# Optimization experiments

Measured on AMD Instinct MI355X. Metric: run time of the kernel, lower is better.

## Reference

```python
import jax, jax.numpy as jnp
import numpy as np

N = 4194304   # variable nodes
M = 2097152   # check nodes
DC = 10       # max check degree


def setup_inputs() -> dict:
    key = jax.random.key(0)
    k1, k2 = jax.random.split(key)
    cn_adj = jax.random.randint(k1, (M, DC), 0, N, dtype=jnp.int32)
    # pad: last neighbor slot of every other check is empty (-1)
    cn_adj = cn_adj.at[:, -1].set(jnp.where(jnp.arange(M) % 2 == 0, -1, cn_adj[:, -1]))
    llr0 = jax.random.normal(k2, (N,), jnp.float32)
    gamma = jnp.ones((), jnp.float32)  # learnable scaling (learn_gamma=True)
    return {"llr0": llr0, "gamma": gamma, "cn_adj": cn_adj, "n_iter": 5}


def _bp(llr0, gamma, cn_adj, n_iter):
    n = llr0.shape[0]
    valid = cn_adj >= 0
    # original gathers v2c[cn_adj] with raw -1 entries -> numpy-style wrap to index n-1
    gather_idx = jnp.where(valid, cn_adj, n - 1)
    # original masks padded slots out of the scatter-add only
    scatter_idx = jnp.where(valid, cn_adj, 0)

    def bp_step(v2c, _):
        msgs = v2c[gather_idx]                               # (M, DC) gather
        sign = jnp.prod(jnp.sign(msgs + 1e-12), axis=1)      # (M,)
        mag = jnp.min(jnp.abs(msgs), axis=1)                 # (M,) min-sum magnitude
        c2v = gamma * sign * mag                             # (M,) scaled min-sum
        msg = jnp.where(valid, c2v[:, None], 0.0)            # mask padded edges
        v_sum = jnp.zeros(n, llr0.dtype).at[scatter_idx].add(msg)  # scatter-add to variables
        return llr0 + v_sum - v2c, None

    v2c0 = jnp.zeros(n, llr0.dtype)
    v2c_final, _ = jax.lax.scan(bp_step, v2c0, None, length=n_iter)
    return llr0 + v2c_final


def reference(llr0, gamma, cn_adj, n_iter):
    return _bp(llr0, gamma, cn_adj, n_iter)
```

## Files before the change

kernel.cpp:

```cpp
#include <hip/hip_runtime.h>
#include <hip/hip_fp16.h>

#define DCC 10
#define NB 2048
#define NBLK 256
#define HTHREADS 1024

typedef int iv4 __attribute__((ext_vector_type(4)));


__global__ __launch_bounds__(256) void bp_init2_kernel(
    const float* __restrict__ llr0, float* __restrict__ v2c,
    unsigned short* __restrict__ v2c_h, int Nq) {
  int i = blockIdx.x * blockDim.x + threadIdx.x;
  if (i >= Nq) return;
  float4 l = reinterpret_cast<const float4*>(llr0)[i];
  reinterpret_cast<float4*>(v2c)[i] = l;
  reinterpret_cast<__half2*>(v2c_h)[2 * i]     = __floats2half2_rn(l.x, l.y);
  reinterpret_cast<__half2*>(v2c_h)[2 * i + 1] = __floats2half2_rn(l.z, l.w);
}

__global__ __launch_bounds__(HTHREADS) void bp_hist_kernel(
    const int* __restrict__ adj, unsigned* __restrict__ hist,
    int i4_per_block, int i4_total) {
  __shared__ unsigned h[NB];
  for (int i = threadIdx.x; i < NB; i += HTHREADS) h[i] = 0u;
  __syncthreads();
  const iv4* p = reinterpret_cast<const iv4*>(adj);
  int base = blockIdx.x * i4_per_block;
  int lim = base + i4_per_block;
  if (lim > i4_total) lim = i4_total;
  for (int g = base + (int)threadIdx.x; g < lim; g += HTHREADS) {
    iv4 r = __builtin_nontemporal_load(p + g);
    if (r.x >= 0) atomicAdd(&h[(unsigned)r.x >> 11], 1u);
    if (r.y >= 0) atomicAdd(&h[(unsigned)r.y >> 11], 1u);
    if (r.z >= 0) atomicAdd(&h[(unsigned)r.z >> 11], 1u);
    if (r.w >= 0) atomicAdd(&h[(unsigned)r.w >> 11], 1u);
  }
  __syncthreads();
  for (int i = threadIdx.x; i < NB; i += HTHREADS)
    hist[(size_t)i * NBLK + blockIdx.x] = h[i];
}

__global__ __launch_bounds__(256) void bp_scan1_kernel(
    unsigned* __restrict__ data, unsigned* __restrict__ sums) {
  __shared__ unsigned ts[256];
  const int base = blockIdx.x * 1024;
  uint4 d = reinterpret_cast<const uint4*>(data + base)[threadIdx.x];
  unsigned tsum = d.x + d.y + d.z + d.w;
  ts[threadIdx.x] = tsum;
  __syncthreads();
  for (int off = 1; off < 256; off <<= 1) {
    unsigned add = ((int)threadIdx.x >= off) ? ts[threadIdx.x - off] : 0u;
    __syncthreads();
    ts[threadIdx.x] += add;
    __syncthreads();
  }
  unsigned run = ts[threadIdx.x] - tsum;
  if (threadIdx.x == 255) sums[blockIdx.x] = ts[255];
  uint4 o;
  o.x = run; run += d.x;
  o.y = run; run += d.y;
  o.z = run; run += d.z;
  o.w = run;
  reinterpret_cast<uint4*>(data + base)[threadIdx.x] = o;
}

__global__ __launch_bounds__(256) void bp_scan2_kernel(
    unsigned* __restrict__ sums, unsigned* __restrict__ total_p, int n) {
  __shared__ unsigned ts[256];
  __shared__ unsigned carry_s;
  if (threadIdx.x == 0) carry_s = 0u;
  __syncthreads();
  for (int c = 0; c < n; c += 256) {
    int idx = c + (int)threadIdx.x;
    unsigned orig = (idx < n) ? sums[idx] : 0u;
    ts[threadIdx.x] = orig;
    __syncthreads();
    for (int off = 1; off < 256; off <<= 1) {
      unsigned add = ((int)threadIdx.x >= off) ? ts[threadIdx.x - off] : 0u;
      __syncthreads();
      ts[threadIdx.x] += add;
      __syncthreads();
    }
    unsigned excl = ts[threadIdx.x] - orig + carry_s;
    if (idx < n) sums[idx] = excl;
    __syncthreads();
    if (threadIdx.x == 0) carry_s += ts[255];
    __syncthreads();
  }
  if (threadIdx.x == 0) *total_p = carry_s;
}

__global__ __launch_bounds__(HTHREADS) void bp_sortscatter_kernel(
    const int* __restrict__ adj, const unsigned* __restrict__ hist_s,
    const unsigned* __restrict__ sums_s, unsigned* __restrict__ recs,
    int i4_per_block, int i4_total) {
  __shared__ unsigned gstart[NB];
  __shared__ unsigned cnt[NB];
  __shared__ unsigned flushed[NB];
  __shared__ unsigned buf[NB * 8];
  for (int i = threadIdx.x; i < NB; i += HTHREADS) {
    unsigned idx = (unsigned)i * NBLK + blockIdx.x;
    gstart[i] = hist_s[idx] + sums_s[idx >> 10];
    cnt[i] = 0u;
    flushed[i] = 0u;
  }
  __syncthreads();
  const iv4* p = reinterpret_cast<const iv4*>(adj);
  int base = blockIdx.x * i4_per_block;
  int lim = base + i4_per_block;
  if (lim > i4_total) lim = i4_total;
  for (int ph = base; ph < lim; ph += HTHREADS) {
    int g = ph + (int)threadIdx.x;
    if (g < lim) {
      iv4 r = __builtin_nontemporal_load(p + g);
      int s4 = g * 4;
      int av[4] = {r.x, r.y, r.z, r.w};
#pragma unroll
      for (int j = 0; j < 4; ++j) {
        int ai = av[j];
        if (ai >= 0) {
          unsigned bin = (unsigned)ai >> 11;
          unsigned rec =
              ((unsigned)(ai & (NB - 1)) << 21) | ((unsigned)(s4 + j) / DCC);
          unsigned pos = atomicAdd(&cnt[bin], 1u);
          if (pos < flushed[bin] + 8u)
            buf[bin * 8 + (pos & 7u)] = rec;
          else
            recs[gstart[bin] + pos] = rec;
        }
      }
    }
    __syncthreads();
    for (int b = threadIdx.x; b < NB; b += HTHREADS) {
      unsigned c = cnt[b], f = flushed[b];
      if (c - f >= 8u) {
        unsigned gp = gstart[b] + f;
#pragma unroll
        for (int k = 0; k < 8; ++k) recs[gp + k] = buf[b * 8 + ((f + k) & 7u)];
        flushed[b] = c;
      }
    }
    __syncthreads();
  }
  for (int b = threadIdx.x; b < NB; b += HTHREADS) {
    unsigned c = cnt[b], f = flushed[b], gp = gstart[b];
    for (unsigned q = f; q < c; ++q) recs[gp + q] = buf[b * 8 + (q & 7u)];
  }
}

__global__ __launch_bounds__(256) void bp_gather1_kernel(
    const int* __restrict__ adj, const unsigned short* __restrict__ v2c_h,
    unsigned* __restrict__ state, int Mhalf, int N, int lo, int hi) {
  int t = blockIdx.x * blockDim.x + threadIdx.x;
  if (t >= Mhalf) return;
  const iv4* p = reinterpret_cast<const iv4*>(adj + (size_t)t * 2 * DCC);
  iv4 r0 = __builtin_nontemporal_load(p);
  iv4 r1 = __builtin_nontemporal_load(p + 1);
  iv4 r2 = __builtin_nontemporal_load(p + 2);
  iv4 r3 = __builtin_nontemporal_load(p + 3);
  iv4 r4 = __builtin_nontemporal_load(p + 4);
  int a[20] = {r0.x, r0.y, r0.z, r0.w, r1.x, r1.y, r1.z, r1.w,
               r2.x, r2.y, r2.z, r2.w, r3.x, r3.y, r3.z, r3.w,
               r4.x, r4.y, r4.z, r4.w};
  unsigned s2[2];
#pragma unroll
  for (int c = 0; c < 2; ++c) {
    unsigned sgn = 0u;
    unsigned mab = 0x7c00u;
#pragma unroll
    for (int j = 0; j < DCC; ++j) {
      int ai = a[c * DCC + j];
      int gi = (ai >= 0) ? ai : (N - 1);
      if (gi >= lo && gi < hi) {
        unsigned hb = (unsigned)v2c_h[gi];
        unsigned ab = hb & 0x7fffu;
        sgn ^= (ab != 0u) ? (hb & 0x8000u) : 0u;
        mab = (ab < mab) ? ab : mab;
      }
    }
    s2[c] = mab | sgn;
  }
  state[t] = s2[0] | (s2[1] << 16);
}

__global__ __launch_bounds__(256) void bp_gather2_kernel(
    const int* __restrict__ adj, const unsigned short* __restrict__ v2c_h,
    const unsigned* __restrict__ state0, unsigned short* __restrict__ c2v_h,
    const float* __restrict__ gamma_p, int Mhalf, int N, int lo, int hi) {
  int t = blockIdx.x * blockDim.x + threadIdx.x;
  if (t >= Mhalf) return;
  const float gamma = *gamma_p;
  const iv4* p = reinterpret_cast<const iv4*>(adj + (size_t)t * 2 * DCC);
  iv4 r0 = __builtin_nontemporal_load(p);
  iv4 r1 = __builtin_nontemporal_load(p + 1);
  iv4 r2 = __builtin_nontemporal_load(p + 2);
  iv4 r3 = __builtin_nontemporal_load(p + 3);
  iv4 r4 = __builtin_nontemporal_load(p + 4);
  int a[20] = {r0.x, r0.y, r0.z, r0.w, r1.x, r1.y, r1.z, r1.w,
               r2.x, r2.y, r2.z, r2.w, r3.x, r3.y, r3.z, r3.w,
               r4.x, r4.y, r4.z, r4.w};
  unsigned p0 = state0[t];
  unsigned outw = 0u;
#pragma unroll
  for (int c = 0; c < 2; ++c) {
    unsigned sgn = 0u;
    unsigned mab = 0x7c00u;
#pragma unroll
    for (int j = 0; j < DCC; ++j) {
      int ai = a[c * DCC + j];
      int gi = (ai >= 0) ? ai : (N - 1);
      if (gi >= lo && gi < hi) {
        unsigned hb = (unsigned)v2c_h[gi];
        unsigned ab = hb & 0x7fffu;
        sgn ^= (ab != 0u) ? (hb & 0x8000u) : 0u;
        mab = (ab < mab) ? ab : mab;
      }
    }
    unsigned q0 = (c == 0) ? (p0 & 0xffffu) : (p0 >> 16);
    unsigned a0 = q0 & 0x7fffu;
    unsigned ab = (a0 < mab) ? a0 : mab;
    unsigned sg = ((q0 ^ sgn) & 0x8000u);
    float val = gamma * __half2float(__ushort_as_half((unsigned short)ab));
    val = __uint_as_float(__float_as_uint(val) ^ (sg << 16));
    outw |= ((unsigned)__half_as_ushort(__float2half_rn(val))) << (16 * c);
  }
  reinterpret_cast<unsigned*>(c2v_h)[t] = outw;
}

__global__ __launch_bounds__(256) void bp_accvar_kernel(
    const unsigned* __restrict__ recs, const unsigned short* __restrict__ c2v_h,
    const unsigned* __restrict__ hist_s, const unsigned* __restrict__ sums_s,
    const unsigned* __restrict__ total_p, const float* __restrict__ llr0,
    float* __restrict__ v2c, unsigned short* __restrict__ v2c_h,
    float* __restrict__ out) {
  __shared__ __align__(16) float acc[NB];
  const int b = blockIdx.x;
  for (int i = threadIdx.x; i < NB; i += 256) acc[i] = 0.0f;
  unsigned i0 = (unsigned)b * NBLK;
  unsigned start = hist_s[i0] + sums_s[i0 >> 10];
  unsigned end = (b == NB - 1)
                     ? *total_p
                     : (hist_s[i0 + NBLK] + sums_s[(i0 + NBLK) >> 10]);
  __syncthreads();
  for (unsigned e = start + threadIdx.x; e < end; e += 256) {
    unsigned rec = recs[e];
    float val = __half2float(__ushort_as_half(c2v_h[rec & 0x1FFFFFu]));
    atomicAdd(&acc[rec >> 21], val);
  }
  __syncthreads();
  const int gq = b * (NB / 4);
#pragma unroll
  for (int k = 0; k < 2; ++k) {
    int li = k * 256 + (int)threadIdx.x;
    int gi = gq + li;
    float4 l = reinterpret_cast<const float4*>(llr0)[gi];
    float4 v = reinterpret_cast<float4*>(v2c)[gi];
    float4 s = reinterpret_cast<const float4*>(acc)[li];
    float4 nv;
    nv.x = l.x + s.x - v.x;
    nv.y = l.y + s.y - v.y;
    nv.z = l.z + s.z - v.z;
    nv.w = l.w + s.w - v.w;
    if (out != nullptr) {
      float4 o;
      o.x = l.x + nv.x;
      o.y = l.y + nv.y;
      o.z = l.z + nv.z;
      o.w = l.w + nv.w;
      reinterpret_cast<float4*>(out)[gi] = o;
    } else {
      reinterpret_cast<float4*>(v2c)[gi] = nv;
      reinterpret_cast<__half2*>(v2c_h)[2 * gi]     = __floats2half2_rn(nv.x, nv.y);
      reinterpret_cast<__half2*>(v2c_h)[2 * gi + 1] = __floats2half2_rn(nv.z, nv.w);
    }
  }
}


__global__ __launch_bounds__(256) void bp_init_kernel(
    const float* __restrict__ llr0, float* __restrict__ v2c,
    float* __restrict__ vsum, __half* __restrict__ v2c_h, int Nq) {
  int i = blockIdx.x * blockDim.x + threadIdx.x;
  if (i >= Nq) return;
  float4 l = reinterpret_cast<const float4*>(llr0)[i];
  reinterpret_cast<float4*>(v2c)[i] = l;
  reinterpret_cast<float4*>(vsum)[i] = make_float4(0.f, 0.f, 0.f, 0.f);
  reinterpret_cast<__half2*>(v2c_h)[2 * i]     = __floats2half2_rn(l.x, l.y);
  reinterpret_cast<__half2*>(v2c_h)[2 * i + 1] = __floats2half2_rn(l.z, l.w);
}

__global__ __launch_bounds__(256) void bp_check_kernel(
    const int* __restrict__ adj, const __half* __restrict__ v2c_h,
    float* __restrict__ vsum, const float* __restrict__ gamma_p,
    int Mhalf, int N) {
  int t = blockIdx.x * blockDim.x + threadIdx.x;
  if (t >= Mhalf) return;
  const float gamma = *gamma_p;
  const int4* p = reinterpret_cast<const int4*>(adj + (size_t)t * 2 * DCC);
  int4 r0 = p[0], r1 = p[1], r2 = p[2], r3 = p[3], r4 = p[4];
  int a[20] = {r0.x, r0.y, r0.z, r0.w, r1.x, r1.y, r1.z, r1.w,
               r2.x, r2.y, r2.z, r2.w, r3.x, r3.y, r3.z, r3.w,
               r4.x, r4.y, r4.z, r4.w};
#pragma unroll
  for (int c = 0; c < 2; ++c) {
    unsigned sgnbits = 0u;
    float mag = 3.402823466e+38f;
#pragma unroll
    for (int j = 0; j < DCC; ++j) {
      int ai = a[c * DCC + j];
      int gi = (ai >= 0) ? ai : (N - 1);
      float v = __half2float(v2c_h[gi]);
      sgnbits ^= (__float_as_uint(v + 1e-12f) & 0x80000000u);
      mag = fminf(mag, fabsf(v));
    }
    float c2v = __uint_as_float(__float_as_uint(gamma * mag) ^ sgnbits);
#pragma unroll
    for (int j = 0; j < DCC; ++j) {
      int ai = a[c * DCC + j];
      if (ai >= 0) unsafeAtomicAdd(&vsum[ai], c2v);
    }
  }
}

__global__ __launch_bounds__(256) void bp_var_kernel(
    const float* __restrict__ llr0, float* __restrict__ v2c,
    float* __restrict__ vsum, __half* __restrict__ v2c_h,
    float* __restrict__ out, int Nq) {
  int i = blockIdx.x * blockDim.x + threadIdx.x;
  if (i >= Nq) return;
  float4 l = reinterpret_cast<const float4*>(llr0)[i];
  float4 v = reinterpret_cast<float4*>(v2c)[i];
  float4 s = reinterpret_cast<float4*>(vsum)[i];
  float4 nv;
  nv.x = l.x + s.x - v.x;
  nv.y = l.y + s.y - v.y;
  nv.z = l.z + s.z - v.z;
  nv.w = l.w + s.w - v.w;
  reinterpret_cast<float4*>(v2c)[i] = nv;
  reinterpret_cast<float4*>(vsum)[i] = make_float4(0.f, 0.f, 0.f, 0.f);
  reinterpret_cast<__half2*>(v2c_h)[2 * i]     = __floats2half2_rn(nv.x, nv.y);
  reinterpret_cast<__half2*>(v2c_h)[2 * i + 1] = __floats2half2_rn(nv.z, nv.w);
  if (out != nullptr) {
    float4 o;
    o.x = l.x + nv.x;
    o.y = l.y + nv.y;
    o.z = l.z + nv.z;
    o.w = l.w + nv.w;
    reinterpret_cast<float4*>(out)[i] = o;
  }
}


extern "C" void kernel_launch(void* const* d_in, const int* in_sizes, int n_in,
                              void* d_out, int out_size, void* d_ws, size_t ws_size,
                              hipStream_t stream) {
  const float* llr0  = (const float*)d_in[0];
  const float* gamma = (const float*)d_in[1];
  const int*   adj   = (const int*)d_in[2];
  const int N = in_sizes[0];
  const int M = in_sizes[2] / DCC;
  const int Mh = M / 2;
  const int NITER = 5;
  const int Nq = N / 4;
  const int varBlocks = (Nq + 255) / 256;
  const int chkBlocks = (Mh + 255) / 256;
  const int Nh = N / 2;

  char* w = (char*)d_ws;
  auto carve = [&](size_t bytes) {
    char* r = w;
    w += (bytes + 255) & ~(size_t)255;
    return r;
  };
  float*          v2c    = (float*)carve((size_t)N * 4);
  unsigned short* v2c_h  = (unsigned short*)carve((size_t)N * 2);
  unsigned*       state0 = (unsigned*)carve((size_t)Mh * 4);
  unsigned short* c2v_h  = (unsigned short*)carve((size_t)M * 2);
  unsigned*       hist   = (unsigned*)carve((size_t)NB * NBLK * 4);
  unsigned*       sums   = (unsigned*)carve((size_t)513 * 4);
  unsigned*       recs   = (unsigned*)carve((size_t)M * DCC * 4);
  unsigned*       total_p = sums + 512;
  size_t need = (size_t)(w - (char*)d_ws);

  const int i4_total = (M * DCC) / 4;
  const int i4_per_block = (i4_total + NBLK - 1) / NBLK;
  const int scanN = (NB * NBLK) / 1024;

  bool fast = (need <= ws_size) && (N == NB * 2048) && (M <= (1 << 21)) &&
              ((M * DCC) % 4 == 0);

  if (fast) {
    bp_init2_kernel<<<varBlocks, 256, 0, stream>>>(llr0, v2c, v2c_h, Nq);
    bp_hist_kernel<<<NBLK, HTHREADS, 0, stream>>>(adj, hist, i4_per_block, i4_total);
    bp_scan1_kernel<<<scanN, 256, 0, stream>>>(hist, sums);
    bp_scan2_kernel<<<1, 256, 0, stream>>>(sums, total_p, scanN);
    bp_sortscatter_kernel<<<NBLK, HTHREADS, 0, stream>>>(adj, hist, sums, recs,
                                                         i4_per_block, i4_total);
    for (int it = 1; it < NITER; ++it) {
      bp_gather1_kernel<<<chkBlocks, 256, 0, stream>>>(
          adj, v2c_h, state0, Mh, N, 0, Nh);
      bp_gather2_kernel<<<chkBlocks, 256, 0, stream>>>(
          adj, v2c_h, state0, c2v_h, gamma, Mh, N, Nh, N);
      float* outp = (it == NITER - 1) ? (float*)d_out : nullptr;
      bp_accvar_kernel<<<NB, 256, 0, stream>>>(
          recs, c2v_h, hist, sums, total_p, llr0, v2c, v2c_h, outp);
    }
  } else {
    float*  fv2c   = (float*)d_ws;
    float*  fvsum  = fv2c + N;
    __half* fv2c_h = (__half*)(fvsum + N);
    bp_init_kernel<<<varBlocks, 256, 0, stream>>>(llr0, fv2c, fvsum, fv2c_h, Nq);
    for (int it = 1; it < NITER; ++it) {
      bp_check_kernel<<<chkBlocks, 256, 0, stream>>>(adj, fv2c_h, fvsum, gamma, Mh, N);
      float* outp = (it == NITER - 1) ? (float*)d_out : nullptr;
      bp_var_kernel<<<varBlocks, 256, 0, stream>>>(llr0, fv2c, fvsum, fv2c_h, outp, Nq);
    }
  }
}
```

Before: 1.337 ms.

## Process four checks per thread, privatize histogram, widen sort buffers

The gather kernels now handle four check nodes per thread instead of two. Each thread loads ten int4 adjacency vectors and writes uint2 state and c2v words, which means fewer threads and wider stores. The histogram kernel splits its shared bins by thread parity to reduce atomic contention. The sort-scatter kernel doubles its per-bin staging buffer to 16 entries and rotates slots by bin index, aiming for longer coalesced flushes and fewer LDS bank conflicts. In exchange, the gather kernels use more registers per thread and fewer threads are available to hide gather latency.

```diff
diff --git a/kernel.cpp b/kernel.cpp
--- a/kernel.cpp
+++ b/kernel.cpp
@@ -23,23 +23,24 @@
 __global__ __launch_bounds__(HTHREADS) void bp_hist_kernel(
     const int* __restrict__ adj, unsigned* __restrict__ hist,
     int i4_per_block, int i4_total) {
-  __shared__ unsigned h[NB];
-  for (int i = threadIdx.x; i < NB; i += HTHREADS) h[i] = 0u;
-  __syncthreads();
+  __shared__ unsigned h[2 * NB];
+  for (int i = threadIdx.x; i < 2 * NB; i += HTHREADS) h[i] = 0u;
+  __syncthreads();
+  const unsigned par = threadIdx.x & 1u;
   const iv4* p = reinterpret_cast<const iv4*>(adj);
   int base = blockIdx.x * i4_per_block;
   int lim = base + i4_per_block;
   if (lim > i4_total) lim = i4_total;
   for (int g = base + (int)threadIdx.x; g < lim; g += HTHREADS) {
     iv4 r = __builtin_nontemporal_load(p + g);
-    if (r.x >= 0) atomicAdd(&h[(unsigned)r.x >> 11], 1u);
-    if (r.y >= 0) atomicAdd(&h[(unsigned)r.y >> 11], 1u);
-    if (r.z >= 0) atomicAdd(&h[(unsigned)r.z >> 11], 1u);
-    if (r.w >= 0) atomicAdd(&h[(unsigned)r.w >> 11], 1u);
+    if (r.x >= 0) atomicAdd(&h[(((unsigned)r.x >> 11) << 1) | par], 1u);
+    if (r.y >= 0) atomicAdd(&h[(((unsigned)r.y >> 11) << 1) | par], 1u);
+    if (r.z >= 0) atomicAdd(&h[(((unsigned)r.z >> 11) << 1) | par], 1u);
+    if (r.w >= 0) atomicAdd(&h[(((unsigned)r.w >> 11) << 1) | par], 1u);
   }
   __syncthreads();
   for (int i = threadIdx.x; i < NB; i += HTHREADS)
-    hist[(size_t)i * NBLK + blockIdx.x] = h[i];
+    hist[(size_t)i * NBLK + blockIdx.x] = h[2 * i] + h[2 * i + 1];
 }
 
 __global__ __launch_bounds__(256) void bp_scan1_kernel(
@@ -99,7 +100,7 @@
   __shared__ unsigned gstart[NB];
   __shared__ unsigned cnt[NB];
   __shared__ unsigned flushed[NB];
-  __shared__ unsigned buf[NB * 8];
+  __shared__ unsigned buf[NB * 16];
   for (int i = threadIdx.x; i < NB; i += HTHREADS) {
     unsigned idx = (unsigned)i * NBLK + blockIdx.x;
     gstart[i] = hist_s[idx] + sums_s[idx >> 10];
@@ -125,8 +126,8 @@
           unsigned rec =
               ((unsigned)(ai & (NB - 1)) << 21) | ((unsigned)(s4 + j) / DCC);
           unsigned pos = atomicAdd(&cnt[bin], 1u);
-          if (pos < flushed[bin] + 8u)
-            buf[bin * 8 + (pos & 7u)] = rec;
+          if (pos < flushed[bin] + 16u)
+            buf[bin * 16 + ((pos + bin) & 15u)] = rec;
           else
             recs[gstart[bin] + pos] = rec;
         }
@@ -135,10 +136,11 @@
     __syncthreads();
     for (int b = threadIdx.x; b < NB; b += HTHREADS) {
       unsigned c = cnt[b], f = flushed[b];
-      if (c - f >= 8u) {
+      if (c - f >= 16u) {
         unsigned gp = gstart[b] + f;
 #pragma unroll
-        for (int k = 0; k < 8; ++k) recs[gp + k] = buf[b * 8 + ((f + k) & 7u)];
+        for (int k = 0; k < 16; ++k)
+          recs[gp + k] = buf[b * 16 + ((f + k + b) & 15u)];
         flushed[b] = c;
       }
     }
@@ -146,27 +148,26 @@
   }
   for (int b = threadIdx.x; b < NB; b += HTHREADS) {
     unsigned c = cnt[b], f = flushed[b], gp = gstart[b];
-    for (unsigned q = f; q < c; ++q) recs[gp + q] = buf[b * 8 + (q & 7u)];
+    for (unsigned q = f; q < c; ++q)
+      recs[gp + q] = buf[b * 16 + ((q + b) & 15u)];
   }
 }
 
 __global__ __launch_bounds__(256) void bp_gather1_kernel(
     const int* __restrict__ adj, const unsigned short* __restrict__ v2c_h,
-    unsigned* __restrict__ state, int Mhalf, int N, int lo, int hi) {
+    uint2* __restrict__ state, int Mq, int N, int lo, int hi) {
   int t = blockIdx.x * blockDim.x + threadIdx.x;
-  if (t >= Mhalf) return;
-  const iv4* p = reinterpret_cast<const iv4*>(adj + (size_t)t * 2 * DCC);
-  iv4 r0 = __builtin_nontemporal_load(p);
-  iv4 r1 = __builtin_nontemporal_load(p + 1);
-  iv4 r2 = __builtin_nontemporal_load(p + 2);
-  iv4 r3 = __builtin_nontemporal_load(p + 3);
-  iv4 r4 = __builtin_nontemporal_load(p + 4);
-  int a[20] = {r0.x, r0.y, r0.z, r0.w, r1.x, r1.y, r1.z, r1.w,
-               r2.x, r2.y, r2.z, r2.w, r3.x, r3.y, r3.z, r3.w,
-               r4.x, r4.y, r4.z, r4.w};
-  unsigned s2[2];
-#pragma unroll
-  for (int c = 0; c < 2; ++c) {
+  if (t >= Mq) return;
+  const iv4* p = reinterpret_cast<const iv4*>(adj + (size_t)t * 4 * DCC);
+  int a[40];
+#pragma unroll
+  for (int k = 0; k < 10; ++k) {
+    iv4 r = __builtin_nontemporal_load(p + k);
+    a[4 * k] = r.x; a[4 * k + 1] = r.y; a[4 * k + 2] = r.z; a[4 * k + 3] = r.w;
+  }
+  unsigned s4[4];
+#pragma unroll
+  for (int c = 0; c < 4; ++c) {
     unsigned sgn = 0u;
     unsigned mab = 0x7c00u;
 #pragma unroll
@@ -180,31 +181,30 @@
         mab = (ab < mab) ? ab : mab;
       }
     }
-    s2[c] = mab | sgn;
-  }
-  state[t] = s2[0] | (s2[1] << 16);
+    s4[c] = mab | sgn;
+  }
+  state[t] = make_uint2(s4[0] | (s4[1] << 16), s4[2] | (s4[3] << 16));
 }
 
 __global__ __launch_bounds__(256) void bp_gather2_kernel(
     const int* __restrict__ adj, const unsigned short* __restrict__ v2c_h,
-    const unsigned* __restrict__ state0, unsigned short* __restrict__ c2v_h,
-    const float* __restrict__ gamma_p, int Mhalf, int N, int lo, int hi) {
+    const uint2* __restrict__ state0, unsigned short* __restrict__ c2v_h,
+    const float* __restrict__ gamma_p, int Mq, int N, int lo, int hi) {
   int t = blockIdx.x * blockDim.x + threadIdx.x;
-  if (t >= Mhalf) return;
+  if (t >= Mq) return;
   const float gamma = *gamma_p;
-  const iv4* p = reinterpret_cast<const iv4*>(adj + (size_t)t * 2 * DCC);
-  iv4 r0 = __builtin_nontemporal_load(p);
-  iv4 r1 = __builtin_nontemporal_load(p + 1);
-  iv4 r2 = __builtin_nontemporal_load(p + 2);
-  iv4 r3 = __builtin_nontemporal_load(p + 3);
-  iv4 r4 = __builtin_nontemporal_load(p + 4);
-  int a[20] = {r0.x, r0.y, r0.z, r0.w, r1.x, r1.y, r1.z, r1.w,
-               r2.x, r2.y, r2.z, r2.w, r3.x, r3.y, r3.z, r3.w,
-               r4.x, r4.y, r4.z, r4.w};
-  unsigned p0 = state0[t];
-  unsigned outw = 0u;
-#pragma unroll
-  for (int c = 0; c < 2; ++c) {
+  const iv4* p = reinterpret_cast<const iv4*>(adj + (size_t)t * 4 * DCC);
+  int a[40];
+#pragma unroll
+  for (int k = 0; k < 10; ++k) {
+    iv4 r = __builtin_nontemporal_load(p + k);
+    a[4 * k] = r.x; a[4 * k + 1] = r.y; a[4 * k + 2] = r.z; a[4 * k + 3] = r.w;
+  }
+  uint2 p0 = state0[t];
+  unsigned q4[4] = {p0.x & 0xffffu, p0.x >> 16, p0.y & 0xffffu, p0.y >> 16};
+  unsigned ow[4];
+#pragma unroll
+  for (int c = 0; c < 4; ++c) {
     unsigned sgn = 0u;
     unsigned mab = 0x7c00u;
 #pragma unroll
@@ -218,15 +218,16 @@
         mab = (ab < mab) ? ab : mab;
       }
     }
-    unsigned q0 = (c == 0) ? (p0 & 0xffffu) : (p0 >> 16);
+    unsigned q0 = q4[c];
     unsigned a0 = q0 & 0x7fffu;
     unsigned ab = (a0 < mab) ? a0 : mab;
     unsigned sg = ((q0 ^ sgn) & 0x8000u);
     float val = gamma * __half2float(__ushort_as_half((unsigned short)ab));
     val = __uint_as_float(__float_as_uint(val) ^ (sg << 16));
-    outw |= ((unsigned)__half_as_ushort(__float2half_rn(val))) << (16 * c);
-  }
-  reinterpret_cast<unsigned*>(c2v_h)[t] = outw;
+    ow[c] = (unsigned)__half_as_ushort(__float2half_rn(val));
+  }
+  reinterpret_cast<uint2*>(c2v_h)[t] =
+      make_uint2(ow[0] | (ow[1] << 16), ow[2] | (ow[3] << 16));
 }
 
 __global__ __launch_bounds__(256) void bp_accvar_kernel(
@@ -362,10 +363,11 @@
   const int N = in_sizes[0];
   const int M = in_sizes[2] / DCC;
   const int Mh = M / 2;
+  const int Mq4 = M / 4;
   const int NITER = 5;
   const int Nq = N / 4;
   const int varBlocks = (Nq + 255) / 256;
-  const int chkBlocks = (Mh + 255) / 256;
+  const int chkBlocks4 = (Mq4 + 255) / 256;
   const int Nh = N / 2;
 
   char* w = (char*)d_ws;
@@ -389,7 +391,7 @@
   const int scanN = (NB * NBLK) / 1024;
 
   bool fast = (need <= ws_size) && (N == NB * 2048) && (M <= (1 << 21)) &&
-              ((M * DCC) % 4 == 0);
+              ((M % 4) == 0) && ((M * DCC) % 4 == 0);
 
   if (fast) {
     bp_init2_kernel<<<varBlocks, 256, 0, stream>>>(llr0, v2c, v2c_h, Nq);
@@ -399,10 +401,10 @@
     bp_sortscatter_kernel<<<NBLK, HTHREADS, 0, stream>>>(adj, hist, sums, recs,
                                                          i4_per_block, i4_total);
     for (int it = 1; it < NITER; ++it) {
-      bp_gather1_kernel<<<chkBlocks, 256, 0, stream>>>(
-          adj, v2c_h, state0, Mh, N, 0, Nh);
-      bp_gather2_kernel<<<chkBlocks, 256, 0, stream>>>(
-          adj, v2c_h, state0, c2v_h, gamma, Mh, N, Nh, N);
+      bp_gather1_kernel<<<chkBlocks4, 256, 0, stream>>>(
+          adj, v2c_h, (uint2*)state0, Mq4, N, 0, Nh);
+      bp_gather2_kernel<<<chkBlocks4, 256, 0, stream>>>(
+          adj, v2c_h, (const uint2*)state0, c2v_h, gamma, Mq4, N, Nh, N);
       float* outp = (it == NITER - 1) ? (float*)d_out : nullptr;
       bp_accvar_kernel<<<NB, 256, 0, stream>>>(
           recs, c2v_h, hist, sums, total_p, llr0, v2c, v2c_h, outp);
@@ -411,6 +413,7 @@
     float*  fv2c   = (float*)d_ws;
     float*  fvsum  = fv2c + N;
     __half* fv2c_h = (__half*)(fvsum + N);
+    const int chkBlocks = (Mh + 255) / 256;
     bp_init_kernel<<<varBlocks, 256, 0, stream>>>(llr0, fv2c, fvsum, fv2c_h, Nq);
     for (int it = 1; it < NITER; ++it) {
       bp_check_kernel<<<chkBlocks, 256, 0, stream>>>(adj, fv2c_h, fvsum, gamma, Mh, N);
```

Result: slower. 1.467 ms (+9.7%).
